# Kernel optimization log

Hardware: AMD Instinct MI355X
Metric: run time of the kernel (lower is better)

Reference implementation:

```python
import jax, jax.numpy as jnp
import numpy as np

V, B, T, D, L, H = 32000, 2, 2048, 1024, 4, 16
HD = D // H            # 64
HID = int(2 * D * 4 / 3)  # 2730 (SwiGLU hidden, computed in BinaryMLP)
EPS = 1e-6


def setup_inputs() -> dict:
    key = jax.random.key(0)
    ks = jax.random.split(key, 16)
    s = 0.02
    return {
        'emb': jax.random.normal(ks[0], (V, D), jnp.float32) * s,
        'Wq':  jax.random.normal(ks[1], (L, D, D), jnp.float32) * s,
        'Wk':  jax.random.normal(ks[2], (L, D, D), jnp.float32) * s,
        'Wv':  jax.random.normal(ks[3], (L, D, D), jnp.float32) * s,
        'Wo':  jax.random.normal(ks[4], (L, D, D), jnp.float32) * s,
        'W1':  jax.random.normal(ks[5], (L, HID, D), jnp.float32) * s,
        'W3':  jax.random.normal(ks[6], (L, HID, D), jnp.float32) * s,
        'W2':  jax.random.normal(ks[7], (L, D, HID), jnp.float32) * s,
        'g1':  jnp.ones((L, D), jnp.float32),
        'g2':  jnp.ones((L, D), jnp.float32),
        'gf':  jnp.ones((D,), jnp.float32),
        'Wlm': jax.random.normal(ks[8], (V, D), jnp.float32) * s,
        'idx': jax.random.randint(ks[9], (B, T), 0, V, jnp.int64),
    }


def bitnet_quant(w):
    # BitNet b1.58: gamma = mean(|W|); ternarize then rescale (STE: identity grad)
    gamma = jnp.maximum(jnp.mean(jnp.abs(w)), 1e-5)
    wq = jnp.clip(jnp.round(w / gamma), -1.0, 1.0) * gamma
    return w + jax.lax.stop_gradient(wq - w)


def rmsnorm(x, g):
    return x * jax.lax.rsqrt(jnp.mean(x * x, axis=-1, keepdims=True) + EPS) * g


def rope_tables(t_len):
    inv_freq = 1.0 / (10000.0 ** (jnp.arange(0, HD, 2, dtype=jnp.float32) / HD))
    t = jnp.arange(t_len, dtype=jnp.float32)
    freqs = jnp.einsum('i,j->ij', t, inv_freq)       # [T, HD/2]
    emb = jnp.concatenate([freqs, freqs], axis=-1)    # [T, HD]
    return jnp.cos(emb), jnp.sin(emb)


def rotate_half(x):
    x1, x2 = x[..., : HD // 2], x[..., HD // 2:]
    return jnp.concatenate([-x2, x1], axis=-1)


def forward(emb, Wq, Wk, Wv, Wo, W1, W2, W3, g1, g2, gf, Wlm, idx):
    x = emb[idx]                                      # [B,T,D]
    cos, sin = rope_tables(T)                         # [T,HD]
    cos = cos[None, None]; sin = sin[None, None]      # [1,1,T,HD]
    causal = jnp.tril(jnp.ones((T, T), bool))[None, None]
    scale = 1.0 / np.sqrt(HD)

    for l in range(L):
        # --- attention ---
        h = rmsnorm(x, g1[l])
        q = jnp.einsum('btd,ed->bte', h, bitnet_quant(Wq[l]))
        k = jnp.einsum('btd,ed->bte', h, bitnet_quant(Wk[l]))
        v = jnp.einsum('btd,ed->bte', h, bitnet_quant(Wv[l]))
        q = q.reshape(B, T, H, HD).transpose(0, 2, 1, 3)  # [B,H,T,HD]
        k = k.reshape(B, T, H, HD).transpose(0, 2, 1, 3)
        v = v.reshape(B, T, H, HD).transpose(0, 2, 1, 3)
        q = q * cos + rotate_half(q) * sin
        k = k * cos + rotate_half(k) * sin
        att = jnp.einsum('bhqd,bhkd->bhqk', q, k) * scale
        att = jnp.where(causal, att, -jnp.inf)
        att = jax.nn.softmax(att, axis=-1)
        y = jnp.einsum('bhqk,bhkd->bhqd', att, v)
        y = y.transpose(0, 2, 1, 3).reshape(B, T, D)
        y = jnp.einsum('btd,ed->bte', y, bitnet_quant(Wo[l]))
        x = x + y
        # --- SwiGLU MLP ---
        h = rmsnorm(x, g2[l])
        a = jnp.einsum('btd,hd->bth', h, bitnet_quant(W1[l]))
        b = jnp.einsum('btd,hd->bth', h, bitnet_quant(W3[l]))
        m = jnp.einsum('bth,dh->btd', jax.nn.silu(a) * b, bitnet_quant(W2[l]))
        x = x + m

    x = rmsnorm(x, gf)
    logits = jnp.einsum('btd,vd->btv', x, Wlm)        # lm_head is plain Linear
    return logits


def reference(emb, Wq, Wk, Wv, Wo, W1, W2, W3, g1, g2, gf, Wlm, idx):
    return forward(emb, Wq, Wk, Wv, Wo, W1, W2, W3, g1, g2, gf, Wlm, idx)
```

## Files before the change

### kernel.cpp

```cpp
#include <hip/hip_runtime.h>

#define TT   2048
#define BBB  2
#define DDD  1024
#define LLL  4
#define HHH  16
#define VVV  32000
#define HIDR 2730
#define HIDP 2816
#define MMM  (BBB*TT)

typedef __bf16 bf16x8 __attribute__((ext_vector_type(8)));
typedef float  f32x4  __attribute__((ext_vector_type(4)));

#define BAR()    asm volatile("s_barrier" ::: "memory")
#define LGKM0()  asm volatile("s_waitcnt lgkmcnt(0)" ::: "memory")
#define VMC(n)   asm volatile("s_waitcnt vmcnt(" #n ")" ::: "memory")
#define SCHED0() __builtin_amdgcn_sched_barrier(0)

__device__ __forceinline__ void gl2lds16(const void* g, void* l) {
  __builtin_amdgcn_global_load_lds((const __attribute__((address_space(1))) void*)g,
                                   (__attribute__((address_space(3))) void*)l, 16, 0, 0);
}

__device__ __forceinline__ f32x4 mfma16(bf16x8 a, bf16x8 b, f32x4 c) {
  return __builtin_amdgcn_mfma_f32_16x16x32_bf16(a, b, c, 0, 0, 0);
}

__device__ __forceinline__ float block_reduce_sum(float v) {
  __shared__ float red[4];
  #pragma unroll
  for (int o = 32; o > 0; o >>= 1) v += __shfl_xor(v, o);
  int w = threadIdx.x >> 6;
  if ((threadIdx.x & 63) == 0) red[w] = v;
  __syncthreads();
  float r = red[0] + red[1] + red[2] + red[3];
  __syncthreads();
  return r;
}

struct QDesc { const float* src; __bf16* dst; int srcR, srcC, dstR, dstC, quant, pad_; };
struct QDescs { QDesc d[29]; };

__global__ __launch_bounds__(256) void reduce_abs_kernel(QDescs qd, float* partial) {
  const QDesc e = qd.d[blockIdx.y];
  size_t n = (size_t)e.srcR * e.srcC;
  float acc = 0.f;
  for (size_t i = (size_t)blockIdx.x * blockDim.x + threadIdx.x; i < n;
       i += (size_t)gridDim.x * blockDim.x)
    acc += fabsf(e.src[i]);
  float s = block_reduce_sum(acc);
  if (threadIdx.x == 0) partial[blockIdx.y * 256 + blockIdx.x] = s;
}

__global__ __launch_bounds__(256) void finalize_gamma_kernel(QDescs qd, const float* partial,
                                                             float* gamma) {
  int m = blockIdx.x;
  float v = partial[m * 256 + threadIdx.x];
  float s = block_reduce_sum(v);
  if (threadIdx.x == 0) {
    float n = (float)((size_t)qd.d[m].srcR * qd.d[m].srcC);
    gamma[m] = fmaxf(s / n, 1e-5f);
  }
}

__global__ __launch_bounds__(256) void quant_kernel(QDescs qd, const float* gamma) {
  const QDesc e = qd.d[blockIdx.y];
  float g = gamma[blockIdx.y];
  for (int row = blockIdx.x; row < e.dstR; row += gridDim.x) {
    for (int c = threadIdx.x; c < e.dstC; c += blockDim.x) {
      __bf16 o;
      if (row < e.srcR && c < e.srcC) {
        float w = e.src[(size_t)row * e.srcC + c];
        if (e.quant) {
          float q = rintf(w / g);
          q = fminf(1.f, fmaxf(-1.f, q));
          o = (__bf16)q;
        } else {
          o = (__bf16)w;
        }
      } else {
        o = (__bf16)0.f;
      }
      e.dst[(size_t)row * e.dstC + c] = o;
    }
  }
}

__global__ void rope_table_kernel(float* cosT, float* sinT) {
  int i = blockIdx.x * 256 + threadIdx.x;
  int t = i >> 5, j = i & 31;
  float inv = powf(10000.0f, -(float)j * (1.0f / 32.0f));
  float ang = (float)t * inv;
  cosT[i] = cosf(ang);
  sinT[i] = sinf(ang);
}

__global__ void idx_mode_kernel(const void* idxv, int* flag) {
  const long long* p = (const long long*)idxv;
  int good = 1;
  for (int i = threadIdx.x; i < (BBB * TT) / 2; i += 256) {
    long long v = p[i];
    if (v < 0 || v >= VVV) good = 0;
  }
  unsigned long long b = __ballot(good);
  __shared__ int r[4];
  if ((threadIdx.x & 63) == 0) r[threadIdx.x >> 6] = (b == ~0ULL) ? 1 : 0;
  __syncthreads();
  if (threadIdx.x == 0) flag[0] = r[0] & r[1] & r[2] & r[3];
}

__global__ __launch_bounds__(256) void gather_kernel(const float* emb, const void* idxv,
                                                     const int* flag, float* x) {
  int tok = blockIdx.x;
  long long id;
  if (flag[0]) id = ((const long long*)idxv)[tok];
  else         id = (long long)((const int*)idxv)[tok];
  const float4* src = (const float4*)(emb + (size_t)id * DDD);
  float4* dst = (float4*)(x + (size_t)tok * DDD);
  dst[threadIdx.x] = src[threadIdx.x];
}

__global__ __launch_bounds__(256) void rmsnorm_kernel(const float* x, const float* g, __bf16* h) {
  int tok = blockIdx.x;
  const float4* xr = (const float4*)(x + (size_t)tok * DDD);
  float4 v = xr[threadIdx.x];
  float ss = v.x * v.x + v.y * v.y + v.z * v.z + v.w * v.w;
  float tot = block_reduce_sum(ss);
  float r = rsqrtf(tot * (1.0f / (float)DDD) + 1e-6f);
  const float4* gr = (const float4*)g;
  float4 gv = gr[threadIdx.x];
  union { __bf16 o[4]; uint2 u2; } pk;
  pk.o[0] = (__bf16)(v.x * r * gv.x);
  pk.o[1] = (__bf16)(v.y * r * gv.y);
  pk.o[2] = (__bf16)(v.z * r * gv.z);
  pk.o[3] = (__bf16)(v.w * r * gv.w);
  *(uint2*)((char*)h + ((size_t)tok * DDD + threadIdx.x * 4) * 2) = pk.u2;
}

__global__ __launch_bounds__(256) void silumul_kernel(const __bf16* ab5, const float* gam1,
                                                      const float* gam3, __bf16* u) {
  int i = blockIdx.x * 256 + threadIdx.x;
  int row = i / (HIDP / 8);
  int c8 = i - row * (HIDP / 8);
  float g1v = gam1[0], g3v = gam3[0];
  bf16x8 av = ((const bf16x8*)ab5)[(size_t)row * (2 * HIDP / 8) + c8];
  bf16x8 bv = ((const bf16x8*)ab5)[(size_t)row * (2 * HIDP / 8) + (HIDP / 8) + c8];
  bf16x8 o;
  #pragma unroll
  for (int j = 0; j < 8; ++j) {
    float fa = (float)av[j] * g1v;
    float s = fa / (1.0f + __expf(-fa));
    o[j] = (__bf16)(s * (float)bv[j] * g3v);
  }
  ((bf16x8*)u)[i] = o;
}

__global__ __launch_bounds__(256) void repack_kernel(const __bf16* qkv, const float* cosT,
                                                     const float* sinT, __bf16* Qp, __bf16* Kp,
                                                     __bf16* Vp) {
  int bh = blockIdx.y;
  int b = bh >> 4, h = bh & 15;
  int t0 = blockIdx.x * 64;
  int r = threadIdx.x >> 2;
  int cq = (threadIdx.x & 3) * 16;
  int t = t0 + r;
  __shared__ __bf16 vt[64][72];
  size_t src = ((size_t)b * TT + t) * 3072 + h * 64;

  #pragma unroll
  for (int which = 0; which < 2; ++which) {
    const __bf16* inp = qkv + (which ? 1024 : 0);
    __bf16* outp = which ? Kp : Qp;
    __bf16 val[16], par[16];
    *(bf16x8*)&val[0] = *(const bf16x8*)(inp + src + cq);
    *(bf16x8*)&val[8] = *(const bf16x8*)(inp + src + cq + 8);
    *(bf16x8*)&par[0] = *(const bf16x8*)(inp + src + (cq ^ 32));
    *(bf16x8*)&par[8] = *(const bf16x8*)(inp + src + (cq ^ 32) + 8);
    __bf16 o[16];
    #pragma unroll
    for (int i2 = 0; i2 < 16; ++i2) {
      int d = cq + i2;
      float c = cosT[t * 32 + (d & 31)];
      float s = sinT[t * 32 + (d & 31)];
      float x0 = (float)val[i2], xp = (float)par[i2];
      float res = (d < 32) ? (x0 * c - xp * s) : (x0 * c + xp * s);
      o[i2] = (__bf16)res;
    }
    *(bf16x8*)(outp + ((size_t)bh * TT + t) * 64 + cq) = *(bf16x8*)&o[0];
    *(bf16x8*)(outp + ((size_t)bh * TT + t) * 64 + cq + 8) = *(bf16x8*)&o[8];
  }

  bf16x8 v0 = *(const bf16x8*)(qkv + 2048 + src + cq);
  bf16x8 v1 = *(const bf16x8*)(qkv + 2048 + src + cq + 8);
  #pragma unroll
  for (int i2 = 0; i2 < 8; ++i2) {
    vt[r][cq + i2] = v0[i2];
    vt[r][cq + 8 + i2] = v1[i2];
  }
  __syncthreads();
  __bf16 ov[16];
  #pragma unroll
  for (int i2 = 0; i2 < 16; ++i2) ov[i2] = vt[cq + i2][r];
  *(bf16x8*)(Vp + ((size_t)bh * 64 + r) * TT + t0 + cq) = *(bf16x8*)&ov[0];
  *(bf16x8*)(Vp + ((size_t)bh * 64 + r) * TT + t0 + cq + 8) = *(bf16x8*)&ov[8];
}

__global__ __launch_bounds__(256) void attn_kernel(const __bf16* __restrict__ Qp,
                                                   const __bf16* __restrict__ Kp,
                                                   const __bf16* __restrict__ Vp,
                                                   __bf16* __restrict__ y) {
  int nwg = gridDim.x * gridDim.y;
  int orig = blockIdx.y * gridDim.x + blockIdx.x;
  int qq = nwg >> 3;
  int swz = (orig & 7) * qq + (orig >> 3);
  int qt = swz % gridDim.x, bh = swz / gridDim.x;

  int b = bh >> 4, h = bh & 15;
  int lane = threadIdx.x & 63, wave = threadIdx.x >> 6;
  int l15 = lane & 15, l4 = lane >> 4;
  int q0 = qt * 128;
  const int ssw = (l15 & 7);
  const int csw = ((lane & 7) ^ (lane >> 3)) * 8;
  const float SC = 0.125f * 1.44269504f;

  __shared__ __bf16 Ks[64 * 64];
  __shared__ __bf16 Vts[64 * 64];
  __shared__ __bf16 Ps[4][32 * 64];

  const __bf16* Qb = Qp + (size_t)bh * TT * 64;
  bf16x8 qf[2][2];
  #pragma unroll
  for (int mf = 0; mf < 2; ++mf)
    #pragma unroll
    for (int kk = 0; kk < 2; ++kk)
      qf[mf][kk] = *(const bf16x8*)(Qb + (size_t)(q0 + wave * 32 + mf * 16 + l15) * 64 +
                                    kk * 32 + l4 * 8);

  const f32x4 z4 = {0.f, 0.f, 0.f, 0.f};
  f32x4 acc[2][4];
  float mrow[2][4], lrow[2][4];
  #pragma unroll
  for (int mf = 0; mf < 2; ++mf)
    #pragma unroll
    for (int j = 0; j < 4; ++j) { mrow[mf][j] = -1e30f; lrow[mf][j] = 0.f; }
  #pragma unroll
  for (int mf = 0; mf < 2; ++mf)
    #pragma unroll
    for (int df = 0; df < 4; ++df) acc[mf][df] = z4;

  int nkt = q0 / 64 + 2;
  for (int kt = 0; kt < nkt; ++kt) {
    int k0 = kt * 64;
    #pragma unroll
    for (int i = 0; i < 2; ++i) {
      int rbase = wave * 16 + i * 8;
      int row = rbase + (lane >> 3);
      gl2lds16(Kp + ((size_t)bh * TT + k0 + row) * 64 + csw, &Ks[rbase * 64]);
      gl2lds16(Vp + ((size_t)bh * 64 + row) * TT + k0 + csw, &Vts[rbase * 64]);
    }
    __syncthreads();

    f32x4 s[2][4];
    #pragma unroll
    for (int mf = 0; mf < 2; ++mf)
      #pragma unroll
      for (int nf = 0; nf < 4; ++nf) s[mf][nf] = z4;
    #pragma unroll
    for (int kk = 0; kk < 2; ++kk) {
      int slot = ((kk * 4 + l4) ^ ssw) * 8;
      bf16x8 kf[4];
      #pragma unroll
      for (int nf = 0; nf < 4; ++nf)
        kf[nf] = *(const bf16x8*)&Ks[(nf * 16 + l15) * 64 + slot];
      #pragma unroll
      for (int mf = 0; mf < 2; ++mf)
        #pragma unroll
        for (int nf = 0; nf < 4; ++nf) s[mf][nf] = mfma16(qf[mf][kk], kf[nf], s[mf][nf]);
    }

    bool domask = (k0 + 63 > q0);
    #pragma unroll
    for (int mf = 0; mf < 2; ++mf) {
      int qrowb = q0 + wave * 32 + mf * 16 + l4 * 4;
      #pragma unroll
      for (int nf = 0; nf < 4; ++nf) {
        int kg = k0 + nf * 16 + l15;
        #pragma unroll
        for (int j = 0; j < 4; ++j) {
          float vv = s[mf][nf][j] * SC;
          if (domask && kg > qrowb + j) vv = -1e30f;
          s[mf][nf][j] = vv;
        }
      }
    }

    float mx_[2][4];
    float exm = -1e30f;
    #pragma unroll
    for (int mf = 0; mf < 2; ++mf)
      #pragma unroll
      for (int j = 0; j < 4; ++j) {
        float mx = fmaxf(fmaxf(s[mf][0][j], s[mf][1][j]), fmaxf(s[mf][2][j], s[mf][3][j]));
        mx = fmaxf(mx, __shfl_xor(mx, 1));
        mx = fmaxf(mx, __shfl_xor(mx, 2));
        mx = fmaxf(mx, __shfl_xor(mx, 4));
        mx = fmaxf(mx, __shfl_xor(mx, 8));
        mx_[mf][j] = mx;
        exm = fmaxf(exm, mx - mrow[mf][j]);
      }
    if (__ballot(exm > 8.0f) != 0ULL) {
      #pragma unroll
      for (int mf = 0; mf < 2; ++mf)
        #pragma unroll
        for (int j = 0; j < 4; ++j) {
          float mnew = fmaxf(mrow[mf][j], mx_[mf][j]);
          float alpha = exp2f(mrow[mf][j] - mnew);
          mrow[mf][j] = mnew;
          lrow[mf][j] *= alpha;
          #pragma unroll
          for (int df = 0; df < 4; ++df) acc[mf][df][j] *= alpha;
        }
    }

    float psum[2][4];
    #pragma unroll
    for (int mf = 0; mf < 2; ++mf)
      #pragma unroll
      for (int j = 0; j < 4; ++j) psum[mf][j] = 0.f;
    #pragma unroll
    for (int mf = 0; mf < 2; ++mf)
      #pragma unroll
      for (int nf = 0; nf < 4; ++nf)
        #pragma unroll
        for (int j = 0; j < 4; ++j) {
          float pp = exp2f(s[mf][nf][j] - mrow[mf][j]);
          psum[mf][j] += pp;
          int prow = mf * 16 + l4 * 4 + j;
          int pcol = nf * 16 + l15;
          Ps[wave][prow * 64 + (pcol ^ ((prow & 7) << 3))] = (__bf16)pp;
        }
    #pragma unroll
    for (int mf = 0; mf < 2; ++mf)
      #pragma unroll
      for (int j = 0; j < 4; ++j) {
        float rs = psum[mf][j];
        rs += __shfl_xor(rs, 1);
        rs += __shfl_xor(rs, 2);
        rs += __shfl_xor(rs, 4);
        rs += __shfl_xor(rs, 8);
        lrow[mf][j] += rs;
      }

    #pragma unroll
    for (int kk = 0; kk < 2; ++kk) {
      int slot = ((kk * 4 + l4) ^ ssw) * 8;
      bf16x8 pf[2], vf[4];
      #pragma unroll
      for (int mf = 0; mf < 2; ++mf)
        pf[mf] = *(const bf16x8*)&Ps[wave][(mf * 16 + l15) * 64 + slot];
      #pragma unroll
      for (int df = 0; df < 4; ++df)
        vf[df] = *(const bf16x8*)&Vts[(df * 16 + l15) * 64 + slot];
      #pragma unroll
      for (int mf = 0; mf < 2; ++mf)
        #pragma unroll
        for (int df = 0; df < 4; ++df) acc[mf][df] = mfma16(pf[mf], vf[df], acc[mf][df]);
    }
    __syncthreads();
  }

  #pragma unroll
  for (int mf = 0; mf < 2; ++mf)
    #pragma unroll
    for (int j = 0; j < 4; ++j) {
      float inv = 1.0f / lrow[mf][j];
      int qg = q0 + wave * 32 + mf * 16 + l4 * 4 + j;
      size_t base = ((size_t)b * TT + qg) * DDD + h * 64;
      #pragma unroll
      for (int df = 0; df < 4; ++df)
        y[base + df * 16 + l15] = (__bf16)(acc[mf][df][j] * inv);
    }
}

template <int MODE>
__global__ __launch_bounds__(256) void gemm_kernel(const __bf16* __restrict__ A,
                                                   const __bf16* __restrict__ Bw, void* Cout,
                                                   const float* Res, const float* gscale,
                                                   int gshift, int M, int N, int K) {
  __shared__ __bf16 As[128 * 64];
  __shared__ __bf16 Bs[128 * 64];
  int nwg = gridDim.x * gridDim.y;
  int orig = blockIdx.y * gridDim.x + blockIdx.x;
  int qq = nwg >> 3;
  int swz = (orig & 7) * qq + (orig >> 3);
  int bx = swz % gridDim.x, by = swz / gridDim.x;
  const int m0 = bx * 128, n0 = by * 128;

  const int lane = threadIdx.x & 63, wave = threadIdx.x >> 6;
  const int wr = wave >> 1, wc = wave & 1;
  const int l15 = lane & 15, l4 = lane >> 4;
  const int ssw = (l15 & 7);
  const int csw = ((lane & 7) ^ (lane >> 3)) * 8;
  const f32x4 z4 = {0.f, 0.f, 0.f, 0.f};
  f32x4 acc[4][4];
  #pragma unroll
  for (int i = 0; i < 4; ++i)
    #pragma unroll
    for (int j = 0; j < 4; ++j) acc[i][j] = z4;

  const int nk = K >> 6;
  for (int kt = 0; kt < nk; ++kt) {
    const int kb = kt << 6;
    #pragma unroll
    for (int i = 0; i < 4; ++i) {
      int rbase = wave * 32 + i * 8;
      int row = rbase + (lane >> 3);
      gl2lds16(A + (size_t)(m0 + row) * K + kb + csw, &As[rbase * 64]);
      gl2lds16(Bw + (size_t)(n0 + row) * K + kb + csw, &Bs[rbase * 64]);
    }
    __syncthreads();
    #pragma unroll
    for (int kk = 0; kk < 2; ++kk) {
      int slot = ((kk * 4 + l4) ^ ssw) * 8;
      bf16x8 af[4], bfr[4];
      #pragma unroll
      for (int mi = 0; mi < 4; ++mi)
        af[mi] = *(const bf16x8*)&As[(wr * 64 + mi * 16 + l15) * 64 + slot];
      #pragma unroll
      for (int ni = 0; ni < 4; ++ni)
        bfr[ni] = *(const bf16x8*)&Bs[(wc * 64 + ni * 16 + l15) * 64 + slot];
      #pragma unroll
      for (int mi = 0; mi < 4; ++mi)
        #pragma unroll
        for (int ni = 0; ni < 4; ++ni) acc[mi][ni] = mfma16(af[mi], bfr[ni], acc[mi][ni]);
    }
    __syncthreads();
  }

  float sc = gscale ? gscale[n0 >> gshift] : 1.0f;
  #pragma unroll
  for (int mi = 0; mi < 4; ++mi)
    #pragma unroll
    for (int ni = 0; ni < 4; ++ni)
      #pragma unroll
      for (int j = 0; j < 4; ++j) {
        int r = m0 + wr * 64 + mi * 16 + l4 * 4 + j;
        int c = n0 + wc * 64 + ni * 16 + l15;
        size_t off = (size_t)r * N + c;
        float v = acc[mi][ni][j] * sc;
        if (MODE == 0) ((__bf16*)Cout)[off] = (__bf16)v;
        else if (MODE == 1) ((float*)Cout)[off] = Res[off] + v;
        else ((float*)Cout)[off] = v;
      }
}

template <int MODE>
__global__ __launch_bounds__(512, 2) void gemm256_kernel(const __bf16* __restrict__ A,
                                                         const __bf16* __restrict__ Bw,
                                                         void* Cout, const float* Res,
                                                         const float* gscale, int gshift,
                                                         int M, int N, int K) {
  __shared__ __bf16 AS[2][2][256 * 32];
  __shared__ __bf16 BS[2][2][256 * 32];
  int nwg = gridDim.x * gridDim.y;
  int orig = blockIdx.y * gridDim.x + blockIdx.x;
  int qq = nwg >> 3;
  int swz = (orig & 7) * qq + (orig >> 3);
  int bx = swz % gridDim.x, by = swz / gridDim.x;
  const int m0 = bx * 256, n0 = by * 256;

  const int tid = threadIdx.x;
  const int lane = tid & 63, w = tid >> 6;
  const int wr = w >> 2, wc = w & 3;
  const int l15 = lane & 15, l4 = lane >> 4;
  const int lsw = (l15 >> 1) & 3;
  const int srow = w * 16 + (lane >> 2);
  const int sslot = ((lane & 3) ^ ((lane >> 3) & 3)) * 8;

  f32x4 acc[8][4];
  const f32x4 z4 = {0.f, 0.f, 0.f, 0.f};
  #pragma unroll
  for (int i = 0; i < 8; ++i)
    #pragma unroll
    for (int j = 0; j < 4; ++j) acc[i][j] = z4;

  auto stageA = [&](int b, int kh, int t) {
    const __bf16* g = A + (size_t)(m0 + srow) * K + (size_t)t * 64 + kh * 32 + sslot;
    gl2lds16(g, &AS[b][kh][w * 512]);
    gl2lds16(g + (size_t)128 * K, &AS[b][kh][4096 + w * 512]);
  };
  auto stageB = [&](int b, int kh, int t) {
    const __bf16* g = Bw + (size_t)(n0 + srow) * K + (size_t)t * 64 + kh * 32 + sslot;
    gl2lds16(g, &BS[b][kh][w * 512]);
    gl2lds16(g + (size_t)128 * K, &BS[b][kh][4096 + w * 512]);
  };

  bf16x8 af[4], bq[4];
  auto ldA = [&](int b, int kh, int mh) {
    #pragma unroll
    for (int mi = 0; mi < 4; ++mi) {
      int row = wr * 128 + (mh * 4 + mi) * 16 + l15;
      af[mi] = *(const bf16x8*)&AS[b][kh][row * 32 + ((l4 ^ lsw) * 8)];
    }
  };
  auto ldB = [&](int b, int kh) {
    #pragma unroll
    for (int ni = 0; ni < 4; ++ni) {
      int row = wc * 64 + ni * 16 + l15;
      bq[ni] = *(const bf16x8*)&BS[b][kh][row * 32 + ((l4 ^ lsw) * 8)];
    }
  };
  auto domfma = [&](int mh) {
    __builtin_amdgcn_s_setprio(1);
    #pragma unroll
    for (int mi = 0; mi < 4; ++mi)
      #pragma unroll
      for (int ni = 0; ni < 4; ++ni)
        acc[mh * 4 + mi][ni] = mfma16(af[mi], bq[ni], acc[mh * 4 + mi][ni]);
    __builtin_amdgcn_s_setprio(0);
  };

  const int nk = K >> 6;
  const int niter = nk >> 1;
  stageA(0, 0, 0); stageB(0, 0, 0); stageA(0, 1, 0); stageB(0, 1, 0);
  stageB(1, 0, 1); stageA(1, 0, 1); stageB(1, 1, 1);
  VMC(6); SCHED0();
  BAR();

  for (int j = 0; j < niter; ++j) {
    int t1 = 2 * j + 1;
    int t2 = 2 * j + 2; if (t2 > nk - 1) t2 = nk - 1;
    int t3 = 2 * j + 3; if (t3 > nk - 1) t3 = nk - 1;
    ldB(0, 0); ldA(0, 0, 0);
    stageA(1, 1, t1);
    BAR(); LGKM0(); SCHED0();
    domfma(0);
    BAR();
    ldA(0, 0, 1);
    stageB(0, 0, t2);
    BAR(); LGKM0(); SCHED0();
    domfma(1);
    BAR();
    ldB(0, 1); ldA(0, 1, 0);
    stageA(0, 0, t2);
    BAR(); LGKM0(); SCHED0();
    domfma(0);
    BAR();
    ldA(0, 1, 1);
    VMC(4); SCHED0();
    stageB(0, 1, t2);
    BAR(); LGKM0(); SCHED0();
    domfma(1);
    BAR();
    ldB(1, 0); ldA(1, 0, 0);
    stageA(0, 1, t2);
    BAR(); LGKM0(); SCHED0();
    domfma(0);
    BAR();
    ldA(1, 0, 1);
    stageB(1, 0, t3);
    BAR(); LGKM0(); SCHED0();
    domfma(1);
    BAR();
    ldB(1, 1); ldA(1, 1, 0);
    stageA(1, 0, t3);
    BAR(); LGKM0(); SCHED0();
    domfma(0);
    BAR();
    ldA(1, 1, 1);
    VMC(4); SCHED0();
    stageB(1, 1, t3);
    BAR(); LGKM0(); SCHED0();
    domfma(1);
    BAR();
  }

  float sc = gscale ? gscale[n0 >> gshift] : 1.0f;
  #pragma unroll
  for (int mi = 0; mi < 8; ++mi)
    #pragma unroll
    for (int ni = 0; ni < 4; ++ni)
      #pragma unroll
      for (int j = 0; j < 4; ++j) {
        int r = m0 + wr * 128 + mi * 16 + l4 * 4 + j;
        int c = n0 + wc * 64 + ni * 16 + l15;
        size_t off = (size_t)r * N + c;
        float v = acc[mi][ni][j] * sc;
        if (MODE == 0) ((__bf16*)Cout)[off] = (__bf16)v;
        else if (MODE == 1) ((float*)Cout)[off] = Res[off] + v;
        else __builtin_nontemporal_store(v, &((float*)Cout)[off]);
      }
}

extern "C" void kernel_launch(void* const* d_in, const int* in_sizes, int n_in,
                              void* d_out, int out_size, void* d_ws, size_t ws_size,
                              hipStream_t stream) {
  (void)in_sizes; (void)n_in; (void)out_size; (void)ws_size;
  const float* emb = (const float*)d_in[0];
  const float* Wq  = (const float*)d_in[1];
  const float* Wk  = (const float*)d_in[2];
  const float* Wv  = (const float*)d_in[3];
  const float* Wo  = (const float*)d_in[4];
  const float* W1  = (const float*)d_in[5];
  const float* W3  = (const float*)d_in[6];
  const float* W2  = (const float*)d_in[7];
  const float* g1  = (const float*)d_in[8];
  const float* g2  = (const float*)d_in[9];
  const float* gf  = (const float*)d_in[10];
  const float* Wlm = (const float*)d_in[11];
  const void*  idx = d_in[12];
  float* out = (float*)d_out;

  char* p = (char*)d_ws;
  auto take = [&](size_t bytes) -> char* {
    char* r = p;
    p += (bytes + 255) & ~(size_t)255;
    return r;
  };
  __bf16* WqkvQ = (__bf16*)take((size_t)LLL * 3072 * DDD * 2);
  __bf16* WoQ  = (__bf16*)take((size_t)LLL * DDD * DDD * 2);
  __bf16* W13Q = (__bf16*)take((size_t)LLL * 2 * HIDP * DDD * 2);
  __bf16* W2Q  = (__bf16*)take((size_t)LLL * DDD * HIDP * 2);
  __bf16* WlmB = (__bf16*)take((size_t)VVV * DDD * 2);
  float*  xbuf = (float*)take((size_t)MMM * DDD * 4);
  __bf16* hbuf = (__bf16*)take((size_t)MMM * DDD * 2);
  char*   S    = take(69206016);
  float*  cosT = (float*)take((size_t)TT * 32 * 4);
  float*  sinT = (float*)take((size_t)TT * 32 * 4);
  float*  gamma = (float*)take(128);
  float*  partial = (float*)take(29 * 256 * 4);
  int*    flag = (int*)take(256);

  __bf16* qkv = (__bf16*)(S);
  __bf16* Qp  = (__bf16*)(S + 25165824);
  __bf16* Kp  = (__bf16*)(S + 33554432);
  __bf16* Vp  = (__bf16*)(S + 41943040);
  __bf16* ab5 = (__bf16*)(S);
  __bf16* ub  = (__bf16*)(S + 46137344);

  QDescs qd;
  for (int l = 0; l < LLL; ++l) {
    qd.d[l * 4 + 0] = QDesc{Wq + (size_t)l * DDD * DDD,
                            WqkvQ + (size_t)l * 3072 * DDD, DDD, DDD, DDD, DDD, 1, 0};
    qd.d[l * 4 + 1] = QDesc{Wk + (size_t)l * DDD * DDD,
                            WqkvQ + (size_t)l * 3072 * DDD + (size_t)DDD * DDD,
                            DDD, DDD, DDD, DDD, 1, 0};
    qd.d[l * 4 + 2] = QDesc{Wv + (size_t)l * DDD * DDD,
                            WqkvQ + (size_t)l * 3072 * DDD + (size_t)2 * DDD * DDD,
                            DDD, DDD, DDD, DDD, 1, 0};
    qd.d[l * 4 + 3] = QDesc{Wo + (size_t)l * DDD * DDD, WoQ + (size_t)l * DDD * DDD,
                            DDD, DDD, DDD, DDD, 1, 0};
    qd.d[16 + l] = QDesc{W1 + (size_t)l * HIDR * DDD,
                         W13Q + (size_t)l * 2 * HIDP * DDD,
                         HIDR, DDD, HIDP, DDD, 1, 0};
    qd.d[20 + l] = QDesc{W3 + (size_t)l * HIDR * DDD,
                         W13Q + (size_t)l * 2 * HIDP * DDD + (size_t)HIDP * DDD,
                         HIDR, DDD, HIDP, DDD, 1, 0};
    qd.d[24 + l] = QDesc{W2 + (size_t)l * DDD * HIDR, W2Q + (size_t)l * DDD * HIDP,
                         DDD, HIDR, DDD, HIDP, 1, 0};
  }
  qd.d[28] = QDesc{Wlm, WlmB, VVV, DDD, VVV, DDD, 0, 0};

  reduce_abs_kernel<<<dim3(256, 28), 256, 0, stream>>>(qd, partial);
  finalize_gamma_kernel<<<28, 256, 0, stream>>>(qd, partial, gamma);
  quant_kernel<<<dim3(512, 29), 256, 0, stream>>>(qd, gamma);
  rope_table_kernel<<<(TT * 32) / 256, 256, 0, stream>>>(cosT, sinT);
  idx_mode_kernel<<<1, 256, 0, stream>>>(idx, flag);
  gather_kernel<<<MMM, 256, 0, stream>>>(emb, idx, flag, xbuf);

  for (int l = 0; l < LLL; ++l) {
    rmsnorm_kernel<<<MMM, 256, 0, stream>>>(xbuf, g1 + (size_t)l * DDD, hbuf);
    gemm256_kernel<0><<<dim3(16, 12), 512, 0, stream>>>(
        hbuf, WqkvQ + (size_t)l * 3072 * DDD, qkv, nullptr, gamma + l * 4, 10,
        MMM, 3072, DDD);
    repack_kernel<<<dim3(TT / 64, BBB * HHH), 256, 0, stream>>>(qkv, cosT, sinT, Qp, Kp, Vp);
    attn_kernel<<<dim3(TT / 128, BBB * HHH), 256, 0, stream>>>(Qp, Kp, Vp, hbuf);
    gemm_kernel<1><<<dim3(32, 8), 256, 0, stream>>>(hbuf, WoQ + (size_t)l * DDD * DDD, xbuf,
                                                    xbuf, gamma + l * 4 + 3, 30, MMM, DDD, DDD);
    rmsnorm_kernel<<<MMM, 256, 0, stream>>>(xbuf, g2 + (size_t)l * DDD, hbuf);
    gemm256_kernel<0><<<dim3(16, 2 * HIDP / 256), 512, 0, stream>>>(
        hbuf, W13Q + (size_t)l * 2 * HIDP * DDD, ab5, nullptr, nullptr, 30,
        MMM, 2 * HIDP, DDD);
    silumul_kernel<<<(MMM * HIDP / 8) / 256, 256, 0, stream>>>(ab5, gamma + 16 + l,
                                                               gamma + 20 + l, ub);
    gemm_kernel<1><<<dim3(32, 8), 256, 0, stream>>>(ub, W2Q + (size_t)l * DDD * HIDP, xbuf,
                                                    xbuf, gamma + 24 + l, 30, MMM, DDD, HIDP);
  }
  rmsnorm_kernel<<<MMM, 256, 0, stream>>>(xbuf, gf, hbuf);
  gemm256_kernel<2><<<dim3(16, VVV / 256), 512, 0, stream>>>(hbuf, WlmB, out, nullptr, nullptr,
                                                             30, MMM, VVV, DDD);
}
```

Baseline: 2.144 ms.

## Double-buffer attention K/V tiles and vectorize weight quantization passes

Attention now keeps two LDS buffers for K and V and issues the next tile's global-to-LDS loads before computing on the current tile, so load latency can overlap with the MFMA work. The abs-sum reduction now reads float4, and the ternary quantization kernel handles 8 columns per thread with a precomputed reciprocal gamma and 16-byte bf16 stores. The logits epilogue drops the nontemporal store hint in favour of a plain store. Costs: double the K/V LDS footprint, which may lower occupancy, and a possible change in cache behaviour for the large logits write.

```diff
diff --git a/kernel.cpp b/kernel.cpp
--- a/kernel.cpp
+++ b/kernel.cpp
@@ -44,11 +44,14 @@
 
 __global__ __launch_bounds__(256) void reduce_abs_kernel(QDescs qd, float* partial) {
   const QDesc e = qd.d[blockIdx.y];
-  size_t n = (size_t)e.srcR * e.srcC;
+  size_t n4 = ((size_t)e.srcR * e.srcC) >> 2;
+  const float4* s4 = (const float4*)e.src;
   float acc = 0.f;
-  for (size_t i = (size_t)blockIdx.x * blockDim.x + threadIdx.x; i < n;
-       i += (size_t)gridDim.x * blockDim.x)
-    acc += fabsf(e.src[i]);
+  for (size_t i = (size_t)blockIdx.x * blockDim.x + threadIdx.x; i < n4;
+       i += (size_t)gridDim.x * blockDim.x) {
+    float4 v = s4[i];
+    acc += fabsf(v.x) + fabsf(v.y) + fabsf(v.z) + fabsf(v.w);
+  }
   float s = block_reduce_sum(acc);
   if (threadIdx.x == 0) partial[blockIdx.y * 256 + blockIdx.x] = s;
 }
@@ -66,23 +69,37 @@
 
 __global__ __launch_bounds__(256) void quant_kernel(QDescs qd, const float* gamma) {
   const QDesc e = qd.d[blockIdx.y];
-  float g = gamma[blockIdx.y];
+  float invg = 1.0f / gamma[blockIdx.y];
+  int nc8 = e.dstC >> 3;
   for (int row = blockIdx.x; row < e.dstR; row += gridDim.x) {
-    for (int c = threadIdx.x; c < e.dstC; c += blockDim.x) {
-      __bf16 o;
-      if (row < e.srcR && c < e.srcC) {
-        float w = e.src[(size_t)row * e.srcC + c];
+    const float* srow = e.src + (size_t)row * e.srcC;
+    bf16x8* drow = (bf16x8*)(e.dst + (size_t)row * e.dstC);
+    bool rok = row < e.srcR;
+    for (int c8 = threadIdx.x; c8 < nc8; c8 += 256) {
+      int c = c8 * 8;
+      float w[8];
+      if (rok && c + 8 <= e.srcC) {
+        float2 v01 = *(const float2*)(srow + c);
+        float2 v23 = *(const float2*)(srow + c + 2);
+        float2 v45 = *(const float2*)(srow + c + 4);
+        float2 v67 = *(const float2*)(srow + c + 6);
+        w[0] = v01.x; w[1] = v01.y; w[2] = v23.x; w[3] = v23.y;
+        w[4] = v45.x; w[5] = v45.y; w[6] = v67.x; w[7] = v67.y;
+      } else {
+        #pragma unroll
+        for (int j = 0; j < 8; ++j) w[j] = (rok && c + j < e.srcC) ? srow[c + j] : 0.f;
+      }
+      bf16x8 o;
+      #pragma unroll
+      for (int j = 0; j < 8; ++j) {
         if (e.quant) {
-          float q = rintf(w / g);
-          q = fminf(1.f, fmaxf(-1.f, q));
-          o = (__bf16)q;
+          float q = rintf(w[j] * invg);
+          o[j] = (__bf16)fminf(1.f, fmaxf(-1.f, q));
         } else {
-          o = (__bf16)w;
+          o[j] = (__bf16)w[j];
         }
-      } else {
-        o = (__bf16)0.f;
       }
-      e.dst[(size_t)row * e.dstC + c] = o;
+      drow[c8] = o;
     }
   }
 }
@@ -224,8 +241,8 @@
   const int csw = ((lane & 7) ^ (lane >> 3)) * 8;
   const float SC = 0.125f * 1.44269504f;
 
-  __shared__ __bf16 Ks[64 * 64];
-  __shared__ __bf16 Vts[64 * 64];
+  __shared__ __bf16 Ks[2][64 * 64];
+  __shared__ __bf16 Vts[2][64 * 64];
   __shared__ __bf16 Ps[4][32 * 64];
 
   const __bf16* Qb = Qp + (size_t)bh * TT * 64;
@@ -249,17 +266,27 @@
     #pragma unroll
     for (int df = 0; df < 4; ++df) acc[mf][df] = z4;
 
-  int nkt = q0 / 64 + 2;
-  for (int kt = 0; kt < nkt; ++kt) {
+  auto stage = [&](int kt, int buf) {
     int k0 = kt * 64;
     #pragma unroll
     for (int i = 0; i < 2; ++i) {
       int rbase = wave * 16 + i * 8;
       int row = rbase + (lane >> 3);
-      gl2lds16(Kp + ((size_t)bh * TT + k0 + row) * 64 + csw, &Ks[rbase * 64]);
-      gl2lds16(Vp + ((size_t)bh * 64 + row) * TT + k0 + csw, &Vts[rbase * 64]);
-    }
-    __syncthreads();
+      gl2lds16(Kp + ((size_t)bh * TT + k0 + row) * 64 + csw, &Ks[buf][rbase * 64]);
+      gl2lds16(Vp + ((size_t)bh * 64 + row) * TT + k0 + csw, &Vts[buf][rbase * 64]);
+    }
+  };
+
+  int nkt = q0 / 64 + 2;
+  stage(0, 0);
+  __syncthreads();
+
+  for (int kt = 0; kt < nkt; ++kt) {
+    int k0 = kt * 64;
+    int cur = kt & 1;
+    if (kt + 1 < nkt) stage(kt + 1, cur ^ 1);
+    const __bf16* KsC = Ks[cur];
+    const __bf16* VtsC = Vts[cur];
 
     f32x4 s[2][4];
     #pragma unroll
@@ -272,7 +299,7 @@
       bf16x8 kf[4];
       #pragma unroll
       for (int nf = 0; nf < 4; ++nf)
-        kf[nf] = *(const bf16x8*)&Ks[(nf * 16 + l15) * 64 + slot];
+        kf[nf] = *(const bf16x8*)&KsC[(nf * 16 + l15) * 64 + slot];
       #pragma unroll
       for (int mf = 0; mf < 2; ++mf)
         #pragma unroll
@@ -361,7 +388,7 @@
         pf[mf] = *(const bf16x8*)&Ps[wave][(mf * 16 + l15) * 64 + slot];
       #pragma unroll
       for (int df = 0; df < 4; ++df)
-        vf[df] = *(const bf16x8*)&Vts[(df * 16 + l15) * 64 + slot];
+        vf[df] = *(const bf16x8*)&VtsC[(df * 16 + l15) * 64 + slot];
       #pragma unroll
       for (int mf = 0; mf < 2; ++mf)
         #pragma unroll
@@ -589,7 +616,7 @@
         float v = acc[mi][ni][j] * sc;
         if (MODE == 0) ((__bf16*)Cout)[off] = (__bf16)v;
         else if (MODE == 1) ((float*)Cout)[off] = Res[off] + v;
-        else __builtin_nontemporal_store(v, &((float*)Cout)[off]);
+        else ((float*)Cout)[off] = v;
       }
 }
 
```

After: 2.001 ms. 1.07x faster.
